# Kernel tuning notes

Hardware: AMD Instinct MI355X
Metric: run time of the kernel (lower is better)

Reference implementation:

```python
import jax, jax.numpy as jnp
import numpy as np

N_RAYS, N_SAMPLES = 4096, 64
N_HARM_XYZ, N_HARM_DIR = 10, 4
H_XYZ, H_DIR = 256, 128
N_LAYERS_XYZ = 8
SKIPS = (3,)
EMB_XYZ = N_HARM_XYZ * 2 * 3 + 3  # 63
EMB_DIR = N_HARM_DIR * 2 * 3 + 3  # 27


def harmonic(x, n_harmonics):
    freqs = 2.0 ** jnp.arange(n_harmonics, dtype=x.dtype)
    emb = (x[..., None] * freqs).reshape(*x.shape[:-1], -1)
    return jnp.concatenate([jnp.sin(emb), jnp.cos(emb), x], axis=-1)


def _linear_params(key, out_dim, in_dim):
    kw, kb = jax.random.split(key)
    s = 1.0 / np.sqrt(in_dim)
    W = jax.random.uniform(kw, (out_dim, in_dim), jnp.float32, -s, s)
    b = jax.random.uniform(kb, (out_dim,), jnp.float32, -s, s)
    return W, b


def setup_inputs() -> dict:
    key = jax.random.key(0)
    keys = jax.random.split(key, 16)
    inp = {
        'sample_points': jax.random.normal(keys[0], (N_RAYS, N_SAMPLES, 3), jnp.float32),
        'directions': jax.random.normal(keys[1], (N_RAYS, 3), jnp.float32),
    }
    # xyz MLP: layer 0: EMB_XYZ->H; layer i (i>=1): input H, or H+EMB_XYZ if (i-1) in SKIPS
    for i in range(N_LAYERS_XYZ):
        if i == 0:
            in_dim = EMB_XYZ
        elif (i - 1) in SKIPS:
            in_dim = H_XYZ + EMB_XYZ
        else:
            in_dim = H_XYZ
        W, b = _linear_params(keys[2 + i], H_XYZ, in_dim)
        inp[f'Wx{i}'], inp[f'bx{i}'] = W, b
    inp['Wd0'], inp['bd0'] = _linear_params(keys[10], H_DIR, H_XYZ + EMB_DIR)
    inp['Wden'], inp['bden'] = _linear_params(keys[11], 1, H_XYZ)
    inp['Wfeat'], inp['bfeat'] = _linear_params(keys[12], H_XYZ, H_XYZ)
    inp['Wrgb'], inp['brgb'] = _linear_params(keys[13], 3, H_DIR)
    return inp


def reference(sample_points, directions,
              Wx0, bx0, Wx1, bx1, Wx2, bx2, Wx3, bx3,
              Wx4, bx4, Wx5, bx5, Wx6, bx6, Wx7, bx7,
              Wd0, bd0, Wden, bden, Wfeat, bfeat, Wrgb, brgb):
    emb_x = harmonic(sample_points, N_HARM_XYZ)  # [N, S, 63]
    layers = [(Wx0, bx0), (Wx1, bx1), (Wx2, bx2), (Wx3, bx3),
              (Wx4, bx4), (Wx5, bx5), (Wx6, bx6), (Wx7, bx7)]
    x = emb_x
    for i, (W, b) in enumerate(layers):
        x = jax.nn.relu(jnp.einsum('nsi,oi->nso', x, W) + b)
        if i in SKIPS:
            x = jnp.concatenate([x, emb_x], axis=-1)
    density = jax.nn.relu(jnp.einsum('nsi,oi->nso', x, Wden) + bden)  # [N, S, 1]
    x = jax.nn.relu(jnp.einsum('nsi,oi->nso', x, Wfeat) + bfeat)
    dirs = jnp.broadcast_to(directions[:, None, :], (directions.shape[0], x.shape[1], 3))
    emb_d = harmonic(dirs, N_HARM_DIR)  # [N, S, 27]
    x = jnp.concatenate([x, emb_d], axis=-1)
    x = jax.nn.relu(jnp.einsum('nsi,oi->nso', x, Wd0) + bd0)
    rgb = jax.nn.sigmoid(jnp.einsum('nsi,oi->nso', x, Wrgb) + brgb)  # [N, S, 3]
    return jnp.concatenate([density, rgb], axis=-1)  # [N, S, 4]
```

## Files before the change

### kernel.cpp

```cpp
#include <hip/hip_runtime.h>
#include <hip/hip_bf16.h>
#include <math.h>

#define N_RAYS 4096
#define N_SAMPLES 64
#define M_TOTAL (N_RAYS * N_SAMPLES)
#define MTILE 128
#define NBLK (M_TOTAL / MTILE)
#define THREADS 512

#define OFF_W0 0
#define OFF_W1 16384
#define OFF_W2 81920
#define OFF_W3 147456
#define OFF_W4 212992
#define OFF_W5 294912
#define OFF_W6 360448
#define OFF_W7 425984
#define OFF_WF 491520
#define OFF_WD 557056

typedef __attribute__((ext_vector_type(8))) short bf16x8;
typedef __attribute__((ext_vector_type(4))) float f32x4;

__device__ __forceinline__ unsigned short f2bf(float f) {
  union { float f; unsigned u; } v; v.f = f;
  unsigned r = v.u + 0x7FFFu + ((v.u >> 16) & 1u);
  return (unsigned short)(r >> 16);
}
__device__ __forceinline__ float bf2f(unsigned short h) {
  union { unsigned u; float f; } v; v.u = ((unsigned)h) << 16;
  return v.f;
}

template<int STRIDE, int SWL>
__device__ __forceinline__ int sidx(int r, int c) {
  const int f = (r & 7) ^ ((r >> 3) & 1);
  const int cc = (c < SWL) ? (c ^ (f << 3)) : c;
  return r * STRIDE + cc;
}

template<int KPAD, int NF, int SI, int SWLI, int SO, int SWLO>
__device__ __forceinline__ void layer_mfma(
    const unsigned short* __restrict__ inb, int col0,
    unsigned short* __restrict__ outb,
    const unsigned short* __restrict__ W,
    const float* __restrict__ bias,
    int wave, int ln15, int lhi)
{
  f32x4 acc[8][NF];
#pragma unroll
  for (int m = 0; m < 8; ++m)
#pragma unroll
    for (int n = 0; n < NF; ++n)
      acc[m][n] = (f32x4){0.f, 0.f, 0.f, 0.f};

  const unsigned short* wr[NF];
#pragma unroll
  for (int n = 0; n < NF; ++n)
    wr[n] = W + (wave * (NF * 16) + n * 16 + ln15) * KPAD + lhi * 8;

  const int kb = col0 + lhi * 8;
#pragma unroll
  for (int k0 = 0; k0 < KPAD; k0 += 32) {
    bf16x8 b[NF];
#pragma unroll
    for (int n = 0; n < NF; ++n)
      b[n] = *(const bf16x8*)(wr[n] + k0);
#pragma unroll
    for (int g = 0; g < 2; ++g) {
      bf16x8 a[4];
#pragma unroll
      for (int mm = 0; mm < 4; ++mm)
        a[mm] = *(const bf16x8*)(inb + sidx<SI, SWLI>((g * 4 + mm) * 16 + ln15, kb + k0));
#pragma unroll
      for (int n = 0; n < NF; ++n)
#pragma unroll
        for (int mm = 0; mm < 4; ++mm)
          acc[g * 4 + mm][n] =
              __builtin_amdgcn_mfma_f32_16x16x32_bf16(a[mm], b[n], acc[g * 4 + mm][n], 0, 0, 0);
    }
  }

#pragma unroll
  for (int n = 0; n < NF; ++n) {
    const int col = wave * (NF * 16) + n * 16 + ln15;
    const float bb = bias[col];
#pragma unroll
    for (int m = 0; m < 8; ++m) {
      const int r0 = m * 16 + lhi * 4;
#pragma unroll
      for (int r = 0; r < 4; ++r) {
        float v = acc[m][n][r] + bb;
        v = fmaxf(v, 0.f);
        outb[sidx<SO, SWLO>(r0 + r, col)] = f2bf(v);
      }
    }
  }
}

struct NerfArgs {
  const float *sp, *dirs;
  const unsigned short* wp;
  const float *bx0, *bx1, *bx2, *bx3, *bx4, *bx5, *bx6, *bx7;
  const float *bd0, *Wden, *bden, *bfeat, *Wrgb, *brgb;
  float* out;
};

__global__ void __attribute__((amdgpu_flat_work_group_size(THREADS, THREADS),
                               amdgpu_waves_per_eu(2, 2)))
nerf_main(NerfArgs A) {
  extern __shared__ unsigned short lds[];
  unsigned short* buf0 = lds;
  unsigned short* buf1 = lds + 128 * 320;
  const int tid = threadIdx.x;
  const int wave = tid >> 6, lane = tid & 63;
  const int ln15 = lane & 15, lhi = lane >> 4;
  const int blk = blockIdx.x;

  {
    const int r = tid & 127, g = tid >> 7;
    if (g < 3) {
      const float x = A.sp[(blk * MTILE + r) * 3 + g];
      buf0[sidx<320, 320>(r, 256 + 60 + g)] = f2bf(x);
#pragma unroll
      for (int f = 0; f < 10; ++f) {
        const float ar = x * (float)(1 << f);
        buf0[sidx<320, 320>(r, 256 + g * 10 + f)]      = f2bf(sinf(ar));
        buf0[sidx<320, 320>(r, 256 + 30 + g * 10 + f)] = f2bf(cosf(ar));
      }
    } else {
      buf0[sidx<320, 320>(r, 319)] = 0;
    }
  }
  __syncthreads();

  const unsigned short* wp = A.wp;
  layer_mfma<64, 2, 320, 320, 288, 256>(buf0, 256, buf1, wp + OFF_W0, A.bx0, wave, ln15, lhi);
  __syncthreads();
  layer_mfma<256, 2, 288, 256, 320, 320>(buf1, 0, buf0, wp + OFF_W1, A.bx1, wave, ln15, lhi);
  __syncthreads();
  layer_mfma<256, 2, 320, 320, 288, 256>(buf0, 0, buf1, wp + OFF_W2, A.bx2, wave, ln15, lhi);
  __syncthreads();
  layer_mfma<256, 2, 288, 256, 320, 320>(buf1, 0, buf0, wp + OFF_W3, A.bx3, wave, ln15, lhi);
  __syncthreads();
  layer_mfma<320, 2, 320, 320, 288, 256>(buf0, 0, buf1, wp + OFF_W4, A.bx4, wave, ln15, lhi);
  __syncthreads();
  layer_mfma<256, 2, 288, 256, 320, 320>(buf1, 0, buf0, wp + OFF_W5, A.bx5, wave, ln15, lhi);
  __syncthreads();
  layer_mfma<256, 2, 320, 320, 288, 256>(buf0, 0, buf1, wp + OFF_W6, A.bx6, wave, ln15, lhi);
  __syncthreads();
  layer_mfma<256, 2, 288, 256, 320, 320>(buf1, 0, buf0, wp + OFF_W7, A.bx7, wave, ln15, lhi);
  __syncthreads();
  layer_mfma<256, 2, 320, 320, 288, 256>(buf0, 0, buf1, wp + OFF_WF, A.bfeat, wave, ln15, lhi);

  {
    const int r = wave * 16 + ln15;
    float s = 0.f;
#pragma unroll
    for (int jj = 0; jj < 8; ++jj) {
      const bf16x8 ch = *(const bf16x8*)(buf0 + sidx<320, 320>(r, lhi * 64 + jj * 8));
#pragma unroll
      for (int e = 0; e < 8; ++e)
        s += bf2f((unsigned short)ch[e]) * A.Wden[lhi * 64 + jj * 8 + e];
    }
    s += __shfl_xor(s, 16);
    s += __shfl_xor(s, 32);
    if (lhi == 0)
      A.out[(blk * MTILE + r) * 4 + 0] = fmaxf(s + A.bden[0], 0.f);
  }
  if (tid < 64) {
    const int j = tid & 31, h = tid >> 5;
    const float* dp = A.dirs + (blk * 2 + h) * 3;
    float val = 0.f;
    if (j < 12)      { int d = j >> 2, f = j & 3;              val = sinf(dp[d] * (float)(1 << f)); }
    else if (j < 24) { int d = (j - 12) >> 2, f = (j - 12) & 3; val = cosf(dp[d] * (float)(1 << f)); }
    else if (j < 27) { val = dp[j - 24]; }
    buf0[sidx<320, 320>(h, 288 + j)] = f2bf(val);
  }
  __syncthreads();
  for (int idx = tid; idx < 128 * 32; idx += THREADS) {
    const int rr = idx >> 5, cc = idx & 31;
    buf1[sidx<288, 256>(rr, 256 + cc)] = buf0[sidx<320, 320>(rr >> 6, 288 + cc)];
  }
  __syncthreads();
  layer_mfma<288, 1, 288, 256, 320, 320>(buf1, 0, buf0, wp + OFF_WD, A.bd0, wave, ln15, lhi);
  __syncthreads();
  {
    const int r = wave * 16 + ln15;
    float s0 = 0.f, s1 = 0.f, s2 = 0.f;
#pragma unroll
    for (int jj = 0; jj < 4; ++jj) {
      const bf16x8 ch = *(const bf16x8*)(buf0 + sidx<320, 320>(r, lhi * 32 + jj * 8));
#pragma unroll
      for (int e = 0; e < 8; ++e) {
        const int k = lhi * 32 + jj * 8 + e;
        const float xv = bf2f((unsigned short)ch[e]);
        s0 += xv * A.Wrgb[k];
        s1 += xv * A.Wrgb[128 + k];
        s2 += xv * A.Wrgb[256 + k];
      }
    }
    s0 += __shfl_xor(s0, 16); s0 += __shfl_xor(s0, 32);
    s1 += __shfl_xor(s1, 16); s1 += __shfl_xor(s1, 32);
    s2 += __shfl_xor(s2, 16); s2 += __shfl_xor(s2, 32);
    if (lhi == 0) {
      float* o = A.out + (blk * MTILE + r) * 4;
      o[1] = 1.f / (1.f + expf(-(s0 + A.brgb[0])));
      o[2] = 1.f / (1.f + expf(-(s1 + A.brgb[1])));
      o[3] = 1.f / (1.f + expf(-(s2 + A.brgb[2])));
    }
  }
}

struct PackDesc { const float* src; int out_dim, in_dim, kpad, dst_off; };
struct PackArgs { PackDesc d[10]; };

__global__ void __launch_bounds__(256) pack_weights(PackArgs P, unsigned short* dst) {
  const PackDesc pd = P.d[blockIdx.y];
  const int idx = blockIdx.x * 256 + threadIdx.x;
  const int tot = pd.out_dim * pd.kpad;
  if (idx >= tot) return;
  const int o = idx / pd.kpad;
  const int k = idx - o * pd.kpad;
  const float v = (k < pd.in_dim) ? pd.src[o * pd.in_dim + k] : 0.f;
  dst[pd.dst_off + idx] = f2bf(v);
}

extern "C" void kernel_launch(void* const* d_in, const int* in_sizes, int n_in,
                              void* d_out, int out_size, void* d_ws, size_t ws_size,
                              hipStream_t stream) {
  unsigned short* wpack = (unsigned short*)d_ws;

  const float* Wx[8]; const float* bx[8];
  for (int i = 0; i < 8; ++i) {
    Wx[i] = (const float*)d_in[2 + 2 * i];
    bx[i] = (const float*)d_in[3 + 2 * i];
  }

  PackArgs P;
  P.d[0] = { Wx[0], 256, 63, 64, OFF_W0 };
  P.d[1] = { Wx[1], 256, 256, 256, OFF_W1 };
  P.d[2] = { Wx[2], 256, 256, 256, OFF_W2 };
  P.d[3] = { Wx[3], 256, 256, 256, OFF_W3 };
  P.d[4] = { Wx[4], 256, 319, 320, OFF_W4 };
  P.d[5] = { Wx[5], 256, 256, 256, OFF_W5 };
  P.d[6] = { Wx[6], 256, 256, 256, OFF_W6 };
  P.d[7] = { Wx[7], 256, 256, 256, OFF_W7 };
  P.d[8] = { (const float*)d_in[22], 256, 256, 256, OFF_WF };
  P.d[9] = { (const float*)d_in[18], 128, 283, 288, OFF_WD };
  hipLaunchKernelGGL(pack_weights, dim3(320, 10), dim3(256), 0, stream, P, wpack);

  NerfArgs A;
  A.sp = (const float*)d_in[0];
  A.dirs = (const float*)d_in[1];
  A.wp = wpack;
  A.bx0 = bx[0]; A.bx1 = bx[1]; A.bx2 = bx[2]; A.bx3 = bx[3];
  A.bx4 = bx[4]; A.bx5 = bx[5]; A.bx6 = bx[6]; A.bx7 = bx[7];
  A.bd0 = (const float*)d_in[19];
  A.Wden = (const float*)d_in[20];
  A.bden = (const float*)d_in[21];
  A.bfeat = (const float*)d_in[23];
  A.Wrgb = (const float*)d_in[24];
  A.brgb = (const float*)d_in[25];
  A.out = (float*)d_out;

  const int lds_bytes = (128 * 320 + 128 * 288) * 2;
  hipFuncSetAttribute((const void*)nerf_main, hipFuncAttributeMaxDynamicSharedMemorySize, lds_bytes);
  hipLaunchKernelGGL(nerf_main, dim3(NBLK), dim3(THREADS), lds_bytes, stream, A);
}
```

Measured before the change: 547.5 us.

## Halve row tile to 64, swap MFMA operands for vectorized epilogue stores, raise occupancy

The per-block row tile drops from 128 to 64 and the waves-per-EU hint rises from 2 to 4, so more workgroups can be resident and hide latency. MFMA operands are swapped so each lane holds four consecutive output features, which allows vector bias loads and packed 4-wide bf16 LDS stores. The density and rgb results are combined into one float4 global store, and the direction embedding now covers a single ray per block. In exchange, each weight fetch from global/L2 is reused over half as many rows, doubling total weight traffic.

New measurement: 824.3 us. +50.6%, slower.

```diff
diff --git a/kernel.cpp b/kernel.cpp
--- a/kernel.cpp
+++ b/kernel.cpp
@@ -5,7 +5,7 @@
 #define N_RAYS 4096
 #define N_SAMPLES 64
 #define M_TOTAL (N_RAYS * N_SAMPLES)
-#define MTILE 128
+#define MTILE 64
 #define NBLK (M_TOTAL / MTILE)
 #define THREADS 512
 
@@ -22,6 +22,7 @@
 
 typedef __attribute__((ext_vector_type(8))) short bf16x8;
 typedef __attribute__((ext_vector_type(4))) float f32x4;
+typedef __attribute__((ext_vector_type(4))) unsigned short u16x4;
 
 __device__ __forceinline__ unsigned short f2bf(float f) {
   union { float f; unsigned u; } v; v.f = f;
@@ -48,9 +49,9 @@
     const float* __restrict__ bias,
     int wave, int ln15, int lhi)
 {
-  f32x4 acc[8][NF];
-#pragma unroll
-  for (int m = 0; m < 8; ++m)
+  f32x4 acc[4][NF];
+#pragma unroll
+  for (int m = 0; m < 4; ++m)
 #pragma unroll
     for (int n = 0; n < NF; ++n)
       acc[m][n] = (f32x4){0.f, 0.f, 0.f, 0.f};
@@ -63,38 +64,34 @@
   const int kb = col0 + lhi * 8;
 #pragma unroll
   for (int k0 = 0; k0 < KPAD; k0 += 32) {
-    bf16x8 b[NF];
+    bf16x8 w[NF];
 #pragma unroll
     for (int n = 0; n < NF; ++n)
-      b[n] = *(const bf16x8*)(wr[n] + k0);
-#pragma unroll
-    for (int g = 0; g < 2; ++g) {
-      bf16x8 a[4];
-#pragma unroll
-      for (int mm = 0; mm < 4; ++mm)
-        a[mm] = *(const bf16x8*)(inb + sidx<SI, SWLI>((g * 4 + mm) * 16 + ln15, kb + k0));
-#pragma unroll
-      for (int n = 0; n < NF; ++n)
-#pragma unroll
-        for (int mm = 0; mm < 4; ++mm)
-          acc[g * 4 + mm][n] =
-              __builtin_amdgcn_mfma_f32_16x16x32_bf16(a[mm], b[n], acc[g * 4 + mm][n], 0, 0, 0);
-    }
+      w[n] = *(const bf16x8*)(wr[n] + k0);
+    bf16x8 a[4];
+#pragma unroll
+    for (int m = 0; m < 4; ++m)
+      a[m] = *(const bf16x8*)(inb + sidx<SI, SWLI>(m * 16 + ln15, kb + k0));
+#pragma unroll
+    for (int n = 0; n < NF; ++n)
+#pragma unroll
+      for (int m = 0; m < 4; ++m)
+        acc[m][n] = __builtin_amdgcn_mfma_f32_16x16x32_bf16(w[n], a[m], acc[m][n], 0, 0, 0);
   }
 
 #pragma unroll
   for (int n = 0; n < NF; ++n) {
-    const int col = wave * (NF * 16) + n * 16 + ln15;
-    const float bb = bias[col];
-#pragma unroll
-    for (int m = 0; m < 8; ++m) {
-      const int r0 = m * 16 + lhi * 4;
+    const int feat0 = wave * (NF * 16) + n * 16 + lhi * 4;
+    const f32x4 bb = *(const f32x4*)(bias + feat0);
+#pragma unroll
+    for (int m = 0; m < 4; ++m) {
+      u16x4 pk;
 #pragma unroll
       for (int r = 0; r < 4; ++r) {
-        float v = acc[m][n][r] + bb;
-        v = fmaxf(v, 0.f);
-        outb[sidx<SO, SWLO>(r0 + r, col)] = f2bf(v);
+        float v = acc[m][n][r] + bb[r];
+        pk[r] = f2bf(fmaxf(v, 0.f));
       }
+      *(u16x4*)(outb + sidx<SO, SWLO>(m * 16 + ln15, feat0)) = pk;
     }
   }
 }
@@ -108,18 +105,18 @@
 };
 
 __global__ void __attribute__((amdgpu_flat_work_group_size(THREADS, THREADS),
-                               amdgpu_waves_per_eu(2, 2)))
+                               amdgpu_waves_per_eu(4, 4)))
 nerf_main(NerfArgs A) {
   extern __shared__ unsigned short lds[];
   unsigned short* buf0 = lds;
-  unsigned short* buf1 = lds + 128 * 320;
+  unsigned short* buf1 = lds + 64 * 320;
   const int tid = threadIdx.x;
   const int wave = tid >> 6, lane = tid & 63;
   const int ln15 = lane & 15, lhi = lane >> 4;
   const int blk = blockIdx.x;
 
   {
-    const int r = tid & 127, g = tid >> 7;
+    const int r = tid & 63, g = tid >> 6;
     if (g < 3) {
       const float x = A.sp[(blk * MTILE + r) * 3 + g];
       buf0[sidx<320, 320>(r, 256 + 60 + g)] = f2bf(x);
@@ -129,7 +126,7 @@
         buf0[sidx<320, 320>(r, 256 + g * 10 + f)]      = f2bf(sinf(ar));
         buf0[sidx<320, 320>(r, 256 + 30 + g * 10 + f)] = f2bf(cosf(ar));
       }
-    } else {
+    } else if (g == 3) {
       buf0[sidx<320, 320>(r, 319)] = 0;
     }
   }
@@ -154,7 +151,8 @@
   __syncthreads();
   layer_mfma<256, 2, 320, 320, 288, 256>(buf0, 0, buf1, wp + OFF_WF, A.bfeat, wave, ln15, lhi);
 
-  {
+  float dens = 0.f;
+  if (wave < 4) {
     const int r = wave * 16 + ln15;
     float s = 0.f;
 #pragma unroll
@@ -166,27 +164,26 @@
     }
     s += __shfl_xor(s, 16);
     s += __shfl_xor(s, 32);
-    if (lhi == 0)
-      A.out[(blk * MTILE + r) * 4 + 0] = fmaxf(s + A.bden[0], 0.f);
-  }
-  if (tid < 64) {
-    const int j = tid & 31, h = tid >> 5;
-    const float* dp = A.dirs + (blk * 2 + h) * 3;
+    dens = fmaxf(s + A.bden[0], 0.f);
+  }
+  if (tid < 32) {
+    const int j = tid;
+    const float* dp = A.dirs + blk * 3;
     float val = 0.f;
-    if (j < 12)      { int d = j >> 2, f = j & 3;              val = sinf(dp[d] * (float)(1 << f)); }
+    if (j < 12)      { int d = j >> 2, f = j & 3;               val = sinf(dp[d] * (float)(1 << f)); }
     else if (j < 24) { int d = (j - 12) >> 2, f = (j - 12) & 3; val = cosf(dp[d] * (float)(1 << f)); }
     else if (j < 27) { val = dp[j - 24]; }
-    buf0[sidx<320, 320>(h, 288 + j)] = f2bf(val);
-  }
-  __syncthreads();
-  for (int idx = tid; idx < 128 * 32; idx += THREADS) {
+    buf0[sidx<320, 320>(0, 288 + j)] = f2bf(val);
+  }
+  __syncthreads();
+  for (int idx = tid; idx < 64 * 32; idx += THREADS) {
     const int rr = idx >> 5, cc = idx & 31;
-    buf1[sidx<288, 256>(rr, 256 + cc)] = buf0[sidx<320, 320>(rr >> 6, 288 + cc)];
+    buf1[sidx<288, 256>(rr, 256 + cc)] = buf0[sidx<320, 320>(0, 288 + cc)];
   }
   __syncthreads();
   layer_mfma<288, 1, 288, 256, 320, 320>(buf1, 0, buf0, wp + OFF_WD, A.bd0, wave, ln15, lhi);
   __syncthreads();
-  {
+  if (wave < 4) {
     const int r = wave * 16 + ln15;
     float s0 = 0.f, s1 = 0.f, s2 = 0.f;
 #pragma unroll
@@ -205,10 +202,12 @@
     s1 += __shfl_xor(s1, 16); s1 += __shfl_xor(s1, 32);
     s2 += __shfl_xor(s2, 16); s2 += __shfl_xor(s2, 32);
     if (lhi == 0) {
-      float* o = A.out + (blk * MTILE + r) * 4;
+      f32x4 o;
+      o[0] = dens;
       o[1] = 1.f / (1.f + expf(-(s0 + A.brgb[0])));
       o[2] = 1.f / (1.f + expf(-(s1 + A.brgb[1])));
       o[3] = 1.f / (1.f + expf(-(s2 + A.brgb[2])));
+      *(f32x4*)(A.out + (blk * MTILE + r) * 4) = o;
     }
   }
 }
@@ -265,7 +264,7 @@
   A.brgb = (const float*)d_in[25];
   A.out = (float*)d_out;
 
-  const int lds_bytes = (128 * 320 + 128 * 288) * 2;
+  const int lds_bytes = (64 * 320 + 64 * 288) * 2;
   hipFuncSetAttribute((const void*)nerf_main, hipFuncAttributeMaxDynamicSharedMemorySize, lds_bytes);
   hipLaunchKernelGGL(nerf_main, dim3(NBLK), dim3(THREADS), lds_bytes, stream, A);
 }
```

## Swap MFMA operands to write packed 4-wide LDS outputs and vector final store

Applied to the files above, without the earlier changes.

Swaps the A/B operands of the MFMA so each lane's accumulator holds four consecutive output features of one row instead of four rows of one feature. The epilogue can then load the bias as one vector and write four bf16 values with a single 8-byte LDS store instead of four scalar stores. The swizzle is simplified to XOR on row&7, bf16 conversion uses the library intrinsic, and density plus RGB are combined into one 16-byte global store. The risk is new LDS bank conflicts under the simpler swizzle.

Result: faster. 481.8 us (-12.0%).

```diff
diff --git a/kernel.cpp b/kernel.cpp
--- a/kernel.cpp
+++ b/kernel.cpp
@@ -22,11 +22,11 @@
 
 typedef __attribute__((ext_vector_type(8))) short bf16x8;
 typedef __attribute__((ext_vector_type(4))) float f32x4;
+typedef __attribute__((ext_vector_type(4))) unsigned short u16x4;
 
 __device__ __forceinline__ unsigned short f2bf(float f) {
-  union { float f; unsigned u; } v; v.f = f;
-  unsigned r = v.u + 0x7FFFu + ((v.u >> 16) & 1u);
-  return (unsigned short)(r >> 16);
+  __hip_bfloat16 h = __float2bfloat16(f);
+  return *(unsigned short*)&h;
 }
 __device__ __forceinline__ float bf2f(unsigned short h) {
   union { unsigned u; float f; } v; v.u = ((unsigned)h) << 16;
@@ -35,8 +35,7 @@
 
 template<int STRIDE, int SWL>
 __device__ __forceinline__ int sidx(int r, int c) {
-  const int f = (r & 7) ^ ((r >> 3) & 1);
-  const int cc = (c < SWL) ? (c ^ (f << 3)) : c;
+  const int cc = (c < SWL) ? (c ^ ((r & 7) << 3)) : c;
   return r * STRIDE + cc;
 }
 
@@ -63,10 +62,10 @@
   const int kb = col0 + lhi * 8;
 #pragma unroll
   for (int k0 = 0; k0 < KPAD; k0 += 32) {
-    bf16x8 b[NF];
+    bf16x8 w[NF];
 #pragma unroll
     for (int n = 0; n < NF; ++n)
-      b[n] = *(const bf16x8*)(wr[n] + k0);
+      w[n] = *(const bf16x8*)(wr[n] + k0);
 #pragma unroll
     for (int g = 0; g < 2; ++g) {
       bf16x8 a[4];
@@ -78,23 +77,21 @@
 #pragma unroll
         for (int mm = 0; mm < 4; ++mm)
           acc[g * 4 + mm][n] =
-              __builtin_amdgcn_mfma_f32_16x16x32_bf16(a[mm], b[n], acc[g * 4 + mm][n], 0, 0, 0);
+              __builtin_amdgcn_mfma_f32_16x16x32_bf16(w[n], a[mm], acc[g * 4 + mm][n], 0, 0, 0);
     }
   }
 
 #pragma unroll
   for (int n = 0; n < NF; ++n) {
-    const int col = wave * (NF * 16) + n * 16 + ln15;
-    const float bb = bias[col];
+    const int feat0 = wave * (NF * 16) + n * 16 + lhi * 4;
+    const f32x4 bb = *(const f32x4*)(bias + feat0);
 #pragma unroll
     for (int m = 0; m < 8; ++m) {
-      const int r0 = m * 16 + lhi * 4;
-#pragma unroll
-      for (int r = 0; r < 4; ++r) {
-        float v = acc[m][n][r] + bb;
-        v = fmaxf(v, 0.f);
-        outb[sidx<SO, SWLO>(r0 + r, col)] = f2bf(v);
-      }
+      u16x4 pk;
+#pragma unroll
+      for (int r = 0; r < 4; ++r)
+        pk[r] = f2bf(fmaxf(acc[m][n][r] + bb[r], 0.f));
+      *(u16x4*)(outb + sidx<SO, SWLO>(m * 16 + ln15, feat0)) = pk;
     }
   }
 }
@@ -154,6 +151,7 @@
   __syncthreads();
   layer_mfma<256, 2, 320, 320, 288, 256>(buf0, 0, buf1, wp + OFF_WF, A.bfeat, wave, ln15, lhi);
 
+  float dens = 0.f;
   {
     const int r = wave * 16 + ln15;
     float s = 0.f;
@@ -166,14 +164,13 @@
     }
     s += __shfl_xor(s, 16);
     s += __shfl_xor(s, 32);
-    if (lhi == 0)
-      A.out[(blk * MTILE + r) * 4 + 0] = fmaxf(s + A.bden[0], 0.f);
+    dens = fmaxf(s + A.bden[0], 0.f);
   }
   if (tid < 64) {
     const int j = tid & 31, h = tid >> 5;
     const float* dp = A.dirs + (blk * 2 + h) * 3;
     float val = 0.f;
-    if (j < 12)      { int d = j >> 2, f = j & 3;              val = sinf(dp[d] * (float)(1 << f)); }
+    if (j < 12)      { int d = j >> 2, f = j & 3;               val = sinf(dp[d] * (float)(1 << f)); }
     else if (j < 24) { int d = (j - 12) >> 2, f = (j - 12) & 3; val = cosf(dp[d] * (float)(1 << f)); }
     else if (j < 27) { val = dp[j - 24]; }
     buf0[sidx<320, 320>(h, 288 + j)] = f2bf(val);
@@ -205,10 +202,12 @@
     s1 += __shfl_xor(s1, 16); s1 += __shfl_xor(s1, 32);
     s2 += __shfl_xor(s2, 16); s2 += __shfl_xor(s2, 32);
     if (lhi == 0) {
-      float* o = A.out + (blk * MTILE + r) * 4;
+      f32x4 o;
+      o[0] = dens;
       o[1] = 1.f / (1.f + expf(-(s0 + A.brgb[0])));
       o[2] = 1.f / (1.f + expf(-(s1 + A.brgb[1])));
       o[3] = 1.f / (1.f + expf(-(s2 + A.brgb[2])));
+      *(f32x4*)(A.out + (blk * MTILE + r) * 4) = o;
     }
   }
 }
```
